# Kernel tuning notes

Hardware: AMD Instinct MI355X
Metric: run time of the kernel (lower is better)

Reference implementation:

```python
import jax, jax.numpy as jnp
import numpy as np

CUTOFF = 2.0
N_RBF = 16
GAMMA = 10.0
BOX = 8.0


def setup_inputs() -> dict:
    key = jax.random.key(0)
    N, D, K, L = 1024, 128, N_RBF, 3
    ks = jax.random.split(key, 5)
    r = jax.random.uniform(ks[0], (N, 3), dtype=jnp.float32) * BOX
    embed = jax.random.normal(ks[1], (N, D), dtype=jnp.float32) * 0.1
    w_filt = jax.random.normal(ks[2], (L, K, D), dtype=jnp.float32) / np.float32(np.sqrt(K))
    w1 = jax.random.normal(ks[3], (L, D, D), dtype=jnp.float32) / np.float32(np.sqrt(D))
    b1 = jnp.zeros((L, D), dtype=jnp.float32)
    w2 = jax.random.normal(ks[4], (L, D, D), dtype=jnp.float32) / np.float32(np.sqrt(D))
    b2 = jnp.zeros((L, D), dtype=jnp.float32)
    return {"r": r, "embed": embed, "w_filt": w_filt, "w1": w1, "b1": b1, "w2": w2, "b2": b2}


def _edge_features(r):
    # cutoff-based edge construction: all-pairs with cutoff + no-self-edge mask
    N = r.shape[0]
    diff = r[:, None, :] - r[None, :, :]                    # [N,N,3]
    d2 = jnp.sum(diff * diff, axis=-1)                      # [N,N]
    eye = jnp.eye(N, dtype=bool)
    dist = jnp.sqrt(jnp.where(eye, 1.0, d2))                # safe sqrt on diagonal
    mask = (dist < CUTOFF) & (~eye)                         # edge occupancy
    mu = jnp.linspace(0.0, CUTOFF, N_RBF, dtype=jnp.float32)
    rbf = jnp.exp(-GAMMA * (dist[..., None] - mu) ** 2)     # [N,N,K]
    fcut = 0.5 * (jnp.cos(jnp.pi * dist / CUTOFF) + 1.0)    # smooth cutoff envelope
    w = jnp.where(mask, fcut, 0.0)
    return rbf * w[..., None]                               # zero outside cutoff


def reference(r, embed, w_filt, w1, b1, w2, b2):
    rbf = _edge_features(r)                                  # [N,N,K]
    h = embed                                                # initial node embeddings
    L = w_filt.shape[0]
    for l in range(L):
        # per-edge filter (edge update): [N,N,D]
        filt = jnp.einsum('ijk,kd->ijd', rbf, w_filt[l])
        # gather sender features, modulate, scatter-sum to receivers: [N,D]
        agg = jnp.einsum('ijd,jd->id', filt, h)
        # node update (residual MLP)
        m = jax.nn.silu(agg @ w1[l] + b1[l]) @ w2[l] + b2[l]
        h = h + m
    return h
```

## Files before the change

### kernel.cpp

```cpp
#include <hip/hip_runtime.h>
#include <hip/hip_bf16.h>

#define NN 1024
#define DD 128
#define KK 16
#define CAP 128

typedef __attribute__((ext_vector_type(4))) float f32x4;
typedef __attribute__((ext_vector_type(8))) short bf16x8;
typedef __attribute__((ext_vector_type(4))) unsigned int u32x4;

static __device__ __forceinline__ unsigned short f2bf(float x) {
  union { __hip_bfloat16 h; unsigned short u; } v;
  v.h = __float2bfloat16(x);
  return v.u;
}
static __device__ __forceinline__ float bf2f(unsigned short u) {
  union { unsigned int ui; float f; } v;
  v.ui = ((unsigned int)u) << 16;
  return v.f;
}

__global__ __launch_bounds__(256) void edge_build(
    const float* __restrict__ r, const float* __restrict__ embed,
    const float* __restrict__ w1, const float* __restrict__ w2,
    const float* __restrict__ wfilt,
    int* __restrict__ cnt, int* __restrict__ nidx,
    unsigned short* __restrict__ edata16,
    unsigned short* __restrict__ hb16, unsigned short* __restrict__ w1b,
    unsigned short* __restrict__ w2b, unsigned short* __restrict__ wfT)
{
  int b = blockIdx.x, tid = threadIdx.x;
  if (b < 256) {
    __shared__ float Rs[NN][3];
    for (int idx = tid; idx < NN * 3; idx += 256) ((float*)Rs)[idx] = r[idx];
    __syncthreads();
    int wv = tid >> 6, lane = tid & 63;
    int i = b * 4 + wv;
    float xi = Rs[i][0], yi = Rs[i][1], zi = Rs[i][2];
    int base = 0;
    for (int it = 0; it < 16; ++it) {
      int j = it * 64 + lane;
      float dx = xi - Rs[j][0], dy = yi - Rs[j][1], dz = zi - Rs[j][2];
      float d2 = dx * dx + dy * dy + dz * dz;
      bool on = (j != i) && (d2 < 4.0f);
      unsigned long long mask = __ballot(on);
      int slot = base + (int)__popcll(mask & ((1ull << lane) - 1ull));
      if (on && slot < CAP) {
        float dist = sqrtf(d2);
        float w  = 0.5f * (__cosf(1.57079632679f * dist) + 1.0f);
        float E0 = __expf(-10.0f * d2);
        float q  = __expf(2.66666667f * dist);
        float u  = __expf(-0.17777778f);
        float u2 = u * u;
        float p = 1.0f, c = 1.0f, s = u;
        float vals[KK];
        #pragma unroll
        for (int k = 0; k < KK; ++k) {
          vals[k] = w * (E0 * p) * c;
          p *= q; c *= s; s *= u2;
        }
        nidx[i * CAP + slot] = j;
        unsigned short* dst = edata16 + ((size_t)i * CAP + slot) * KK;
        #pragma unroll
        for (int k = 0; k < KK; ++k) dst[k] = f2bf(vals[k]);
      }
      base += (int)__popcll(mask);
    }
    if (lane == 0) cnt[i] = (base < CAP) ? base : CAP;
  } else if (b < 272) {
    int gt = (b - 256) * 256 + tid;
    for (int f = gt; f < 229376; f += 4096) {
      if (f < 131072)      hb16[f]          = f2bf(embed[f]);
      else if (f < 180224) w1b[f - 131072]  = f2bf(w1[f - 131072]);
      else                 w2b[f - 180224]  = f2bf(w2[f - 180224]);
    }
  } else {
    for (int e = tid; e < 3 * 128 * 32; e += 256) {
      int l = e >> 12, rem = e & 4095, dd = rem >> 5, kk = rem & 31;
      wfT[e] = (kk < KK) ? f2bf(wfilt[l * 2048 + kk * 128 + dd])
                         : (unsigned short)0;
    }
  }
}

__global__ __launch_bounds__(256) void layer_fused(
    const int* __restrict__ cnt, const int* __restrict__ nidx,
    const unsigned short* __restrict__ edata16,
    const unsigned short* __restrict__ hb16in,
    const float* __restrict__ hprev,
    const unsigned short* __restrict__ wfTL,
    const unsigned short* __restrict__ w1b, const float* __restrict__ b1,
    const unsigned short* __restrict__ w2b, const float* __restrict__ b2,
    float* __restrict__ hnext,
    unsigned short* __restrict__ hb16out,
    float* __restrict__ outf)
{
  __shared__ unsigned short Hs[64][136];
  __shared__ unsigned short As[64][40];
  __shared__ float xv[128];
  __shared__ float yv[128];
  __shared__ float part4[4][128];

  int i = blockIdx.x, tid = threadIdx.x;
  int w = tid >> 6, lane = tid & 63;
  int lg = lane >> 4, l16 = lane & 15;
  int cn = cnt[i];
  const int* nx = nidx + i * CAP;

  bf16x8 bfr[2];
  #pragma unroll
  for (int nt = 0; nt < 2; ++nt) {
    int d = (w * 2 + nt) * 16 + l16;
    bfr[nt] = *(const bf16x8*)(wfTL + d * 32 + lg * 8);
  }

  float aggv0 = 0.f, aggv1 = 0.f;

  for (int p64 = 0; p64 < cn; p64 += 64) {
    int local_n = cn - p64; if (local_n > 64) local_n = 64;
    __syncthreads();
    #pragma unroll
    for (int it = 0; it < 4; ++it) {
      int c = tid + it * 256;
      int row = c >> 4, ch = c & 15;
      u32x4 v = {0u, 0u, 0u, 0u};
      if (row < local_n) {
        int j = nx[p64 + row];
        v = *(const u32x4*)(hb16in + (size_t)j * DD + ch * 8);
      }
      *(u32x4*)(&Hs[row][ch * 8]) = v;
    }
    {
      int row = tid >> 2, ch = tid & 3;
      u32x4 v = {0u, 0u, 0u, 0u};
      if (row < local_n && ch < 2)
        v = *(const u32x4*)(edata16 + ((size_t)i * CAP + p64 + row) * KK + ch * 8);
      *(u32x4*)(&As[row][ch * 8]) = v;
    }
    __syncthreads();

    bf16x8 af[4];
    #pragma unroll
    for (int mt = 0; mt < 4; ++mt)
      af[mt] = *(const bf16x8*)(&As[mt * 16 + l16][lg * 8]);
    f32x4 acc[4][2];
    #pragma unroll
    for (int mt = 0; mt < 4; ++mt)
      #pragma unroll
      for (int nt = 0; nt < 2; ++nt)
        acc[mt][nt] = (f32x4){0.f, 0.f, 0.f, 0.f};
    #pragma unroll
    for (int mt = 0; mt < 4; ++mt)
      #pragma unroll
      for (int nt = 0; nt < 2; ++nt)
        acc[mt][nt] = __builtin_amdgcn_mfma_f32_16x16x32_bf16(
            af[mt], bfr[nt], acc[mt][nt], 0, 0, 0);

    #pragma unroll
    for (int nt = 0; nt < 2; ++nt) {
      int d = (w * 2 + nt) * 16 + l16;
      float s = 0.f;
      #pragma unroll
      for (int mt = 0; mt < 4; ++mt)
        #pragma unroll
        for (int rr = 0; rr < 4; ++rr)
          s += acc[mt][nt][rr] * bf2f(Hs[mt * 16 + lg * 4 + rr][d]);
      if (nt == 0) aggv0 += s; else aggv1 += s;
    }
  }
  aggv0 += __shfl_xor(aggv0, 16, 64);
  aggv0 += __shfl_xor(aggv0, 32, 64);
  aggv1 += __shfl_xor(aggv1, 16, 64);
  aggv1 += __shfl_xor(aggv1, 32, 64);
  if (lg == 0) {
    xv[(w * 2 + 0) * 16 + l16] = aggv0;
    xv[(w * 2 + 1) * 16 + l16] = aggv1;
  }
  __syncthreads();

  int dp = tid & 63, pp = tid >> 6;
  float o1a = 0.f, o1b = 0.f;
  #pragma unroll 8
  for (int q = 0; q < 32; ++q) {
    int di = pp * 32 + q;
    float x = xv[di];
    unsigned int wp = *(const unsigned int*)(w1b + di * DD + dp * 2);
    o1a += x * bf2f((unsigned short)(wp & 0xffffu));
    o1b += x * bf2f((unsigned short)(wp >> 16));
  }
  part4[pp][dp * 2] = o1a;
  part4[pp][dp * 2 + 1] = o1b;
  __syncthreads();
  if (tid < 128) {
    float x = part4[0][tid] + part4[1][tid] + part4[2][tid] + part4[3][tid] + b1[tid];
    yv[tid] = x / (1.f + __expf(-x));
  }
  __syncthreads();
  float o2a = 0.f, o2b = 0.f;
  #pragma unroll 8
  for (int q = 0; q < 32; ++q) {
    int di = pp * 32 + q;
    float yy = yv[di];
    unsigned int wp = *(const unsigned int*)(w2b + di * DD + dp * 2);
    o2a += yy * bf2f((unsigned short)(wp & 0xffffu));
    o2b += yy * bf2f((unsigned short)(wp >> 16));
  }
  part4[pp][dp * 2] = o2a;
  part4[pp][dp * 2 + 1] = o2b;
  __syncthreads();
  if (tid < 128) {
    float v = part4[0][tid] + part4[1][tid] + part4[2][tid] + part4[3][tid]
              + b2[tid] + hprev[(size_t)i * DD + tid];
    if (outf) {
      outf[(size_t)i * DD + tid] = v;
    } else {
      hnext[(size_t)i * DD + tid]   = v;
      hb16out[(size_t)i * DD + tid] = f2bf(v);
    }
  }
}

extern "C" void kernel_launch(void* const* d_in, const int* in_sizes, int n_in,
                              void* d_out, int out_size, void* d_ws, size_t ws_size,
                              hipStream_t stream) {
  (void)in_sizes; (void)n_in; (void)out_size; (void)ws_size;
  const float* r     = (const float*)d_in[0];
  const float* embed = (const float*)d_in[1];
  const float* wfilt = (const float*)d_in[2];
  const float* w1    = (const float*)d_in[3];
  const float* b1    = (const float*)d_in[4];
  const float* w2    = (const float*)d_in[5];
  const float* b2    = (const float*)d_in[6];

  char* ws = (char*)d_ws;
  size_t off = 0;
  auto alloc = [&](size_t bytes) {
    void* p = ws + off; off += (bytes + 255) & ~(size_t)255; return p;
  };
  unsigned short* EDATA = (unsigned short*)alloc((size_t)NN * CAP * KK * 2);
  int*            NIDX  = (int*)alloc((size_t)NN * CAP * 4);
  int*            CNT   = (int*)alloc((size_t)NN * 4);
  unsigned short* HB16A = (unsigned short*)alloc((size_t)NN * DD * 2);
  unsigned short* HB16B = (unsigned short*)alloc((size_t)NN * DD * 2);
  unsigned short* W1B   = (unsigned short*)alloc((size_t)3 * DD * DD * 2);
  unsigned short* W2B   = (unsigned short*)alloc((size_t)3 * DD * DD * 2);
  unsigned short* WFT   = (unsigned short*)alloc((size_t)3 * DD * 32 * 2);
  float*          HB    = (float*)alloc((size_t)NN * DD * 4);

  edge_build<<<273, 256, 0, stream>>>(r, embed, w1, w2, wfilt,
                                      CNT, NIDX, EDATA, HB16A, W1B, W2B, WFT);

  const float* hp = embed;
  for (int l = 0; l < 3; ++l) {
    bool fin = (l == 2);
    const unsigned short* in16  = (l == 1) ? HB16B : HB16A;
    unsigned short*       out16 = (l == 0) ? HB16B : HB16A;
    layer_fused<<<NN, 256, 0, stream>>>(
        CNT, NIDX, EDATA, in16, hp,
        WFT + (size_t)l * DD * 32,
        W1B + (size_t)l * DD * DD, b1 + (size_t)l * DD,
        W2B + (size_t)l * DD * DD, b2 + (size_t)l * DD,
        fin ? nullptr : HB, fin ? nullptr : out16,
        fin ? (float*)d_out : nullptr);
    hp = HB;
  }
}
```

Baseline: 45.01 us.

## Fuse edge construction with the first message-passing layer into one kernel

Edge building, which was one row per wave across 256 blocks, now runs as one row per block and feeds layer 0 directly in the same kernel. Neighbor indices stay in shared memory, and embeddings and MLP weights are read in fp32 rather than from separately converted bf16 copies. This removes one kernel launch and the global round trip of the edge list before layer 0. The later layers also stage their neighbor index list in shared memory. The cost is that every block now reloads all positions and computes the distances for its row with a per-wave prefix count, which adds redundant work and extra synchronisation.

Result: faster. 43.61 us (-3.1%).

```diff
diff --git a/kernel.cpp b/kernel.cpp
--- a/kernel.cpp
+++ b/kernel.cpp
@@ -20,27 +20,85 @@
   v.ui = ((unsigned int)u) << 16;
   return v.f;
 }
-
-__global__ __launch_bounds__(256) void edge_build(
+static __device__ __forceinline__ unsigned int pack2(float a, float b) {
+  return (unsigned int)f2bf(a) | ((unsigned int)f2bf(b) << 16);
+}
+
+__global__ __launch_bounds__(256) void layer0_full(
     const float* __restrict__ r, const float* __restrict__ embed,
-    const float* __restrict__ w1, const float* __restrict__ w2,
     const float* __restrict__ wfilt,
+    const float* __restrict__ w1, const float* __restrict__ b1,
+    const float* __restrict__ w2, const float* __restrict__ b2,
     int* __restrict__ cnt, int* __restrict__ nidx,
     unsigned short* __restrict__ edata16,
-    unsigned short* __restrict__ hb16, unsigned short* __restrict__ w1b,
-    unsigned short* __restrict__ w2b, unsigned short* __restrict__ wfT)
+    unsigned short* __restrict__ w1ball, unsigned short* __restrict__ w2ball,
+    unsigned short* __restrict__ wfT,
+    float* __restrict__ hnext, unsigned short* __restrict__ hb16out)
 {
   int b = blockIdx.x, tid = threadIdx.x;
-  if (b < 256) {
-    __shared__ float Rs[NN][3];
-    for (int idx = tid; idx < NN * 3; idx += 256) ((float*)Rs)[idx] = r[idx];
-    __syncthreads();
-    int wv = tid >> 6, lane = tid & 63;
-    int i = b * 4 + wv;
-    float xi = Rs[i][0], yi = Rs[i][1], zi = Rs[i][2];
-    int base = 0;
-    for (int it = 0; it < 16; ++it) {
-      int j = it * 64 + lane;
+  if (b >= NN) {
+    if (b < NN + 16) {
+      int gt = (b - NN) * 256 + tid;
+      for (int f = gt; f < 98304; f += 4096) {
+        if (f < 49152) w1ball[f]         = f2bf(w1[f]);
+        else           w2ball[f - 49152] = f2bf(w2[f - 49152]);
+      }
+    } else {
+      for (int e = tid; e < 3 * 128 * 32; e += 256) {
+        int l = e >> 12, rem = e & 4095, dd = rem >> 5, kk = rem & 31;
+        wfT[e] = (kk < KK) ? f2bf(wfilt[l * 2048 + kk * 128 + dd])
+                           : (unsigned short)0;
+      }
+    }
+    return;
+  }
+
+  __shared__ float Rs[NN][3];
+  __shared__ unsigned short Hs[64][136];
+  __shared__ unsigned short As[64][40];
+  __shared__ int   nxs[CAP];
+  __shared__ int   wcnt[4], wbase[4], cn_sh;
+  __shared__ float xv[128];
+  __shared__ float yv[128];
+  __shared__ float part4[4][128];
+
+  int i = b;
+  int w = tid >> 6, lane = tid & 63;
+  int lg = lane >> 4, l16 = lane & 15;
+
+  #pragma unroll
+  for (int it = 0; it < 3; ++it) {
+    int idx = tid + it * 256;
+    ((f32x4*)Rs)[idx] = ((const f32x4*)r)[idx];
+  }
+  __syncthreads();
+
+  float xi = Rs[i][0], yi = Rs[i][1], zi = Rs[i][2];
+
+  int mycount = 0;
+  #pragma unroll
+  for (int it = 0; it < 4; ++it) {
+    int j = w * 256 + it * 64 + lane;
+    float dx = xi - Rs[j][0], dy = yi - Rs[j][1], dz = zi - Rs[j][2];
+    float d2 = dx * dx + dy * dy + dz * dz;
+    bool on = (j != i) && (d2 < 4.0f);
+    mycount += (int)__popcll(__ballot(on));
+  }
+  if (lane == 0) wcnt[w] = mycount;
+  __syncthreads();
+  if (tid == 0) {
+    int acc = 0;
+    #pragma unroll
+    for (int k = 0; k < 4; ++k) { wbase[k] = acc; acc += wcnt[k]; }
+    cn_sh = (acc < CAP) ? acc : CAP;
+  }
+  __syncthreads();
+
+  {
+    int base = wbase[w];
+    #pragma unroll
+    for (int it = 0; it < 4; ++it) {
+      int j = w * 256 + it * 64 + lane;
       float dx = xi - Rs[j][0], dy = yi - Rs[j][1], dz = zi - Rs[j][2];
       float d2 = dx * dx + dy * dy + dz * dz;
       bool on = (j != i) && (d2 < 4.0f);
@@ -48,39 +106,144 @@
       int slot = base + (int)__popcll(mask & ((1ull << lane) - 1ull));
       if (on && slot < CAP) {
         float dist = sqrtf(d2);
-        float w  = 0.5f * (__cosf(1.57079632679f * dist) + 1.0f);
+        float ww = 0.5f * (__cosf(1.57079632679f * dist) + 1.0f);
         float E0 = __expf(-10.0f * d2);
         float q  = __expf(2.66666667f * dist);
         float u  = __expf(-0.17777778f);
         float u2 = u * u;
         float p = 1.0f, c = 1.0f, s = u;
-        float vals[KK];
-        #pragma unroll
-        for (int k = 0; k < KK; ++k) {
-          vals[k] = w * (E0 * p) * c;
-          p *= q; c *= s; s *= u2;
-        }
+        nxs[slot] = j;
         nidx[i * CAP + slot] = j;
         unsigned short* dst = edata16 + ((size_t)i * CAP + slot) * KK;
         #pragma unroll
-        for (int k = 0; k < KK; ++k) dst[k] = f2bf(vals[k]);
+        for (int k = 0; k < KK; ++k) {
+          dst[k] = f2bf(ww * (E0 * p) * c);
+          p *= q; c *= s; s *= u2;
+        }
       }
       base += (int)__popcll(mask);
     }
-    if (lane == 0) cnt[i] = (base < CAP) ? base : CAP;
-  } else if (b < 272) {
-    int gt = (b - 256) * 256 + tid;
-    for (int f = gt; f < 229376; f += 4096) {
-      if (f < 131072)      hb16[f]          = f2bf(embed[f]);
-      else if (f < 180224) w1b[f - 131072]  = f2bf(w1[f - 131072]);
-      else                 w2b[f - 180224]  = f2bf(w2[f - 180224]);
-    }
-  } else {
-    for (int e = tid; e < 3 * 128 * 32; e += 256) {
-      int l = e >> 12, rem = e & 4095, dd = rem >> 5, kk = rem & 31;
-      wfT[e] = (kk < KK) ? f2bf(wfilt[l * 2048 + kk * 128 + dd])
-                         : (unsigned short)0;
-    }
+  }
+  if (tid == 0) cnt[i] = cn_sh;
+  __threadfence_block();
+  __syncthreads();
+  int cn = cn_sh;
+
+  bf16x8 bfr[2];
+  #pragma unroll
+  for (int nt = 0; nt < 2; ++nt) {
+    int d = (w * 2 + nt) * 16 + l16;
+    bf16x8 t = {0,0,0,0,0,0,0,0};
+    if (lg < 2) {
+      #pragma unroll
+      for (int e = 0; e < 8; ++e)
+        t[e] = (short)f2bf(wfilt[(lg * 8 + e) * 128 + d]);
+    }
+    bfr[nt] = t;
+  }
+
+  float aggv0 = 0.f, aggv1 = 0.f;
+  for (int p64 = 0; p64 < cn; p64 += 64) {
+    int local_n = cn - p64; if (local_n > 64) local_n = 64;
+    __syncthreads();
+    #pragma unroll
+    for (int it = 0; it < 4; ++it) {
+      int c = tid + it * 256;
+      int row = c >> 4, ch = c & 15;
+      u32x4 v = {0u, 0u, 0u, 0u};
+      if (row < local_n) {
+        int j = nxs[p64 + row];
+        const float* ep = embed + (size_t)j * DD + ch * 8;
+        f32x4 ea = *(const f32x4*)(ep);
+        f32x4 eb = *(const f32x4*)(ep + 4);
+        v[0] = pack2(ea[0], ea[1]); v[1] = pack2(ea[2], ea[3]);
+        v[2] = pack2(eb[0], eb[1]); v[3] = pack2(eb[2], eb[3]);
+      }
+      *(u32x4*)(&Hs[row][ch * 8]) = v;
+    }
+    {
+      int row = tid >> 2, ch = tid & 3;
+      u32x4 v = {0u, 0u, 0u, 0u};
+      if (row < local_n && ch < 2)
+        v = *(const u32x4*)(edata16 + ((size_t)i * CAP + p64 + row) * KK + ch * 8);
+      *(u32x4*)(&As[row][ch * 8]) = v;
+    }
+    __syncthreads();
+
+    bf16x8 af[4];
+    #pragma unroll
+    for (int mt = 0; mt < 4; ++mt)
+      af[mt] = *(const bf16x8*)(&As[mt * 16 + l16][lg * 8]);
+    f32x4 acc[4][2];
+    #pragma unroll
+    for (int mt = 0; mt < 4; ++mt)
+      #pragma unroll
+      for (int nt = 0; nt < 2; ++nt)
+        acc[mt][nt] = (f32x4){0.f, 0.f, 0.f, 0.f};
+    #pragma unroll
+    for (int mt = 0; mt < 4; ++mt)
+      #pragma unroll
+      for (int nt = 0; nt < 2; ++nt)
+        acc[mt][nt] = __builtin_amdgcn_mfma_f32_16x16x32_bf16(
+            af[mt], bfr[nt], acc[mt][nt], 0, 0, 0);
+
+    #pragma unroll
+    for (int nt = 0; nt < 2; ++nt) {
+      int d = (w * 2 + nt) * 16 + l16;
+      float s = 0.f;
+      #pragma unroll
+      for (int mt = 0; mt < 4; ++mt)
+        #pragma unroll
+        for (int rr = 0; rr < 4; ++rr)
+          s += acc[mt][nt][rr] * bf2f(Hs[mt * 16 + lg * 4 + rr][d]);
+      if (nt == 0) aggv0 += s; else aggv1 += s;
+    }
+  }
+  aggv0 += __shfl_xor(aggv0, 16, 64);
+  aggv0 += __shfl_xor(aggv0, 32, 64);
+  aggv1 += __shfl_xor(aggv1, 16, 64);
+  aggv1 += __shfl_xor(aggv1, 32, 64);
+  if (lg == 0) {
+    xv[(w * 2 + 0) * 16 + l16] = aggv0;
+    xv[(w * 2 + 1) * 16 + l16] = aggv1;
+  }
+  __syncthreads();
+
+  int dp = tid & 63, pp = tid >> 6;
+  float o1a = 0.f, o1b = 0.f;
+  #pragma unroll 8
+  for (int q = 0; q < 32; ++q) {
+    int di = pp * 32 + q;
+    float x = xv[di];
+    float2 wp = *(const float2*)(w1 + di * DD + dp * 2);
+    o1a += x * wp.x;
+    o1b += x * wp.y;
+  }
+  part4[pp][dp * 2] = o1a;
+  part4[pp][dp * 2 + 1] = o1b;
+  __syncthreads();
+  if (tid < 128) {
+    float x = part4[0][tid] + part4[1][tid] + part4[2][tid] + part4[3][tid] + b1[tid];
+    yv[tid] = x / (1.f + __expf(-x));
+  }
+  __syncthreads();
+  float o2a = 0.f, o2b = 0.f;
+  #pragma unroll 8
+  for (int q = 0; q < 32; ++q) {
+    int di = pp * 32 + q;
+    float yy = yv[di];
+    float2 wp = *(const float2*)(w2 + di * DD + dp * 2);
+    o2a += yy * wp.x;
+    o2b += yy * wp.y;
+  }
+  part4[pp][dp * 2] = o2a;
+  part4[pp][dp * 2 + 1] = o2b;
+  __syncthreads();
+  if (tid < 128) {
+    float v = part4[0][tid] + part4[1][tid] + part4[2][tid] + part4[3][tid]
+              + b2[tid] + embed[(size_t)i * DD + tid];
+    hnext[(size_t)i * DD + tid]   = v;
+    hb16out[(size_t)i * DD + tid] = f2bf(v);
   }
 }
 
@@ -98,6 +261,7 @@
 {
   __shared__ unsigned short Hs[64][136];
   __shared__ unsigned short As[64][40];
+  __shared__ int   nxs[CAP];
   __shared__ float xv[128];
   __shared__ float yv[128];
   __shared__ float part4[4][128];
@@ -106,7 +270,6 @@
   int w = tid >> 6, lane = tid & 63;
   int lg = lane >> 4, l16 = lane & 15;
   int cn = cnt[i];
-  const int* nx = nidx + i * CAP;
 
   bf16x8 bfr[2];
   #pragma unroll
@@ -115,8 +278,10 @@
     bfr[nt] = *(const bf16x8*)(wfTL + d * 32 + lg * 8);
   }
 
+  if (tid < CAP) nxs[tid] = nidx[i * CAP + tid];
+  __syncthreads();
+
   float aggv0 = 0.f, aggv1 = 0.f;
-
   for (int p64 = 0; p64 < cn; p64 += 64) {
     int local_n = cn - p64; if (local_n > 64) local_n = 64;
     __syncthreads();
@@ -126,7 +291,7 @@
       int row = c >> 4, ch = c & 15;
       u32x4 v = {0u, 0u, 0u, 0u};
       if (row < local_n) {
-        int j = nx[p64 + row];
+        int j = nxs[p64 + row];
         v = *(const u32x4*)(hb16in + (size_t)j * DD + ch * 8);
       }
       *(u32x4*)(&Hs[row][ch * 8]) = v;
@@ -248,21 +413,20 @@
   unsigned short* WFT   = (unsigned short*)alloc((size_t)3 * DD * 32 * 2);
   float*          HB    = (float*)alloc((size_t)NN * DD * 4);
 
-  edge_build<<<273, 256, 0, stream>>>(r, embed, w1, w2, wfilt,
-                                      CNT, NIDX, EDATA, HB16A, W1B, W2B, WFT);
-
-  const float* hp = embed;
-  for (int l = 0; l < 3; ++l) {
+  layer0_full<<<NN + 17, 256, 0, stream>>>(
+      r, embed, wfilt, w1, b1, w2, b2,
+      CNT, NIDX, EDATA, W1B, W2B, WFT, HB, HB16B);
+
+  for (int l = 1; l < 3; ++l) {
     bool fin = (l == 2);
     const unsigned short* in16  = (l == 1) ? HB16B : HB16A;
-    unsigned short*       out16 = (l == 0) ? HB16B : HB16A;
+    unsigned short*       out16 = (l == 1) ? HB16A : HB16B;
     layer_fused<<<NN, 256, 0, stream>>>(
-        CNT, NIDX, EDATA, in16, hp,
+        CNT, NIDX, EDATA, in16, HB,
         WFT + (size_t)l * DD * 32,
         W1B + (size_t)l * DD * DD, b1 + (size_t)l * DD,
         W2B + (size_t)l * DD * DD, b2 + (size_t)l * DD,
         fin ? nullptr : HB, fin ? nullptr : out16,
         fin ? (float*)d_out : nullptr);
-    hp = HB;
-  }
-}
+  }
+}
```
